# Optimization experiments

Hardware: AMD Instinct MI355X
Metric: run time of the kernel (lower is better)

## Reference

```python
import jax, jax.numpy as jnp
import numpy as np

V = 32000; D = 1024; L = 2; H = 16; KVH = 4; HD = D // H; E = 8; FF = 2048; K = 2
B = 2; S = 1024; WINDOW = 4096; THETA = 10000.0; EPS = 1e-6


def setup_inputs() -> dict:
    key = jax.random.key(0)
    ks = jax.random.split(key, 12)
    std = 0.02
    return {
        'tokens': jax.random.randint(ks[0], (B, S), 0, V),
        'tok_emb': jax.random.normal(ks[1], (V, D), jnp.float32),  # nn.Embedding default N(0,1)
        'norm1_w': jnp.ones((L, D), jnp.float32),
        'norm2_w': jnp.ones((L, D), jnp.float32),
        'wq': jax.random.normal(ks[2], (L, D, D), jnp.float32) * std,
        'wk': jax.random.normal(ks[3], (L, KVH * HD, D), jnp.float32) * std,
        'wv': jax.random.normal(ks[4], (L, KVH * HD, D), jnp.float32) * std,
        'wo': jax.random.normal(ks[5], (L, D, D), jnp.float32) * std,
        'router_w': jax.random.normal(ks[6], (L, E, D), jnp.float32) * (std / np.sqrt(D)),
        'w1': jax.random.normal(ks[7], (L, E, FF, D), jnp.float32) * std,
        'w2': jax.random.normal(ks[8], (L, E, FF, D), jnp.float32) * std,
        'w3': jax.random.normal(ks[9], (L, E, D, FF), jnp.float32) * std,
        'normf_w': jnp.ones((D,), jnp.float32),
        'head_w': jax.random.normal(ks[10], (V, D), jnp.float32) * std,
    }


def rmsnorm(x, w):
    # F.normalize(x, dim=-1, eps) * w * sqrt(d)
    n = jnp.linalg.norm(x, axis=-1, keepdims=True)
    return x / jnp.maximum(n, EPS) * w * np.float32(np.sqrt(x.shape[-1]))


def rope(x, cos, sin):
    # x: (b, s, h, hd); pairs are interleaved (even, odd) per view_as_complex
    x2 = x.reshape(x.shape[:-1] + (-1, 2))
    x0, x1 = x2[..., 0], x2[..., 1]
    o0 = x0 * cos - x1 * sin
    o1 = x0 * sin + x1 * cos
    return jnp.stack([o0, o1], axis=-1).reshape(x.shape)


def attention(x, wq, wk, wv, wo, cos, sin):
    b, s, _ = x.shape
    q = (x @ wq.T).reshape(b, s, H, HD)
    k = (x @ wk.T).reshape(b, s, KVH, HD)
    v = (x @ wv.T).reshape(b, s, KVH, HD)
    q = rope(q, cos, sin)
    k = rope(k, cos, sin)
    g = H // KVH
    k = jnp.repeat(k, g, axis=2)
    v = jnp.repeat(v, g, axis=2)
    scores = jnp.einsum('bqhd,bkhd->bhqk', q, k) / np.float32(np.sqrt(HD))
    i = jnp.arange(s)[:, None]; j = jnp.arange(s)[None, :]
    allow = (j <= i) & (i - j < WINDOW)  # causal + sliding window
    scores = jnp.where(allow, scores, -jnp.inf)
    attn = jax.nn.softmax(scores, axis=-1)
    out = jnp.einsum('bhqk,bkhd->bqhd', attn, v).reshape(b, s, D)
    return out @ wo.T


def moe(x, router_w, w1, w2, w3):
    b, s, d = x.shape
    logits = jnp.einsum('bsd,ed->bse', x, router_w)
    probs = jax.nn.softmax(logits, axis=-1)
    _, idx = jax.lax.top_k(probs, K)                      # (b, s, K)
    mask = jax.nn.one_hot(idx, E, dtype=x.dtype).sum(-2)  # (b, s, E) binary
    xt = x.reshape(-1, d)           # (T, d)
    mt = mask.reshape(-1, E)        # (T, E)
    # Dense masked dispatch: every expert computed on all tokens, combine masks to zero
    u = jnp.einsum('td,efd->etf', xt, w1)
    g = jax.nn.silu(u) * jnp.einsum('td,efd->etf', xt, w2)
    y = jnp.einsum('etf,edf->etd', g, w3)
    out = jnp.einsum('etd,te->td', y, mt).reshape(b, s, d)  # unweighted combine (per source)
    # aux losses
    z_loss = jnp.mean(jax.scipy.special.logsumexp(logits, axis=-1)) ** 2
    load = probs.sum(axis=0)  # (s, E), matching probs.sum(dim=0) in source
    load_loss = (jnp.std(load, ddof=1) / jnp.mean(load)) ** 2
    aux = 0.001 * z_loss + 0.001 * load_loss
    return out, aux


def _rope_tables(dtype):
    freqs = 1.0 / (THETA ** (np.arange(0, HD, 2, dtype=np.float32) / HD))
    ang = np.arange(S, dtype=np.float32)[:, None] * freqs[None, :]
    cos = jnp.asarray(np.cos(ang), dtype)[None, :, None, :]
    sin = jnp.asarray(np.sin(ang), dtype)[None, :, None, :]
    return cos, sin


def reference(tokens, tok_emb, norm1_w, norm2_w, wq, wk, wv, wo, router_w, w1, w2, w3, normf_w, head_w):
    x = tok_emb[tokens]  # (B, S, D)
    cos, sin = _rope_tables(x.dtype)
    attn_scale = np.float32(1.0 / np.sqrt(2.0 * L))
    aux_total = jnp.zeros((), x.dtype)
    for l in range(L):
        x = x + attn_scale * attention(rmsnorm(x, norm1_w[l]), wq[l], wk[l], wv[l], wo[l], cos, sin)
        mo, aux = moe(rmsnorm(x, norm2_w[l]), router_w[l], w1[l], w2[l], w3[l])
        x = x + mo
        aux_total = aux_total + aux
    logits = rmsnorm(x, normf_w) @ head_w.T
    return logits, aux_total
```

## Files before the change

kernel.cpp:

```cpp
#include <hip/hip_runtime.h>
#include <math.h>

#define DEV __device__ __forceinline__

using v8s = __attribute__((ext_vector_type(8))) short;
using v4f = __attribute__((ext_vector_type(4))) float;

DEV short f2bf(float f) {
    unsigned u = __float_as_uint(f);
    unsigned r = (u + 0x7fffu + ((u >> 16) & 1u)) >> 16;
    return (short)(unsigned short)r;
}
DEV float bf2f(short s) {
    return __uint_as_float(((unsigned)(unsigned short)s) << 16);
}

DEV void gload16(const short* g, short* l) {
    __builtin_amdgcn_global_load_lds((const __attribute__((address_space(1))) void*)g,
                                     (__attribute__((address_space(3))) void*)l,
                                     16, 0, 0);
}

DEV float block_sum256(float v, float* red) {
    __syncthreads();
#pragma unroll
    for (int o = 32; o >= 1; o >>= 1) v += __shfl_down(v, o, 64);
    if ((threadIdx.x & 63) == 0) red[threadIdx.x >> 6] = v;
    __syncthreads();
    return red[0] + red[1] + red[2] + red[3];
}
DEV float block_max256(float v, float* red) {
    __syncthreads();
#pragma unroll
    for (int o = 32; o >= 1; o >>= 1) v = fmaxf(v, __shfl_down(v, o, 64));
    if ((threadIdx.x & 63) == 0) red[threadIdx.x >> 6] = v;
    __syncthreads();
    return fmaxf(fmaxf(red[0], red[1]), fmaxf(red[2], red[3]));
}


__global__ __launch_bounds__(256) void conv_kernel(const float* __restrict__ src,
                                                   short* __restrict__ hi, short* __restrict__ lo,
                                                   long total4, long chunk4, long dstStride4) {
    for (long i = (long)blockIdx.x * 256 + threadIdx.x; i < total4; i += (long)gridDim.x * 256) {
        long c = i / chunk4, r = i - c * chunk4;
        long d = c * dstStride4 + r;
        float4 f = ((const float4*)src)[i];
        short h0 = f2bf(f.x), h1 = f2bf(f.y), h2 = f2bf(f.z), h3 = f2bf(f.w);
        ((ushort4*)hi)[d] = make_ushort4((unsigned short)h0, (unsigned short)h1,
                                         (unsigned short)h2, (unsigned short)h3);
        if (lo) {
            short l0 = f2bf(f.x - bf2f(h0)), l1 = f2bf(f.y - bf2f(h1));
            short l2 = f2bf(f.z - bf2f(h2)), l3 = f2bf(f.w - bf2f(h3));
            ((ushort4*)lo)[d] = make_ushort4((unsigned short)l0, (unsigned short)l1,
                                             (unsigned short)l2, (unsigned short)l3);
        }
    }
}

struct GemmP {
    const short* Ah; const short* Al;
    const short* Bh; const short* Bl;
    float* C; short* Ch; short* Cl;
    const int* cnt; const int* prefix; const int* ltok; const int* lrow;
    long strideAz, strideBz, strideCz;
    int M, N, K, lda, ldb, ldc;
    float alpha;
    int outMode;
    int gqaB;
    int attnC;
    int grouped;
    int causalSkip;
    int causalK;
    int ntiles, S, G;
};

template<bool SPLIT>
__global__ __launch_bounds__(256) void gemm_bt(GemmP p) {
    const int lid = blockIdx.x;
    const int xcd = lid & 7, sI = lid >> 3;
    const int gi = xcd + 8 * (sI / p.S);
    if (gi >= p.G) return;
    const int mt = sI % p.S;
    const int nt = gi % p.ntiles;
    const int z  = gi / p.ntiles;
    if (p.causalSkip && nt > mt) return;

    const int tid = threadIdx.x;

    int Mz = p.M;
    const int* ltokz = nullptr; const int* lrowz = nullptr; int pz = 0;
    if (p.grouped) {
        Mz = p.cnt[z]; pz = p.prefix[z];
        ltokz = p.ltok + z * 2048; lrowz = p.lrow + z * 2048;
    }
    if (mt * 128 >= Mz) return;

    long aOff = (long)z * p.strideAz;
    long bOff, cOff;
    if (p.gqaB) { int b = z >> 4, h = z & 15; bOff = (long)(b * 4 + (h >> 2)) * p.strideBz; }
    else bOff = (long)z * p.strideBz;
    if (p.attnC) { int b = z >> 4, h = z & 15; cOff = (long)b * 1048576 + h * 64; }
    else cOff = (long)z * p.strideCz;

    extern __shared__ char smem[];
    short* Ahs = (short*)smem;
    short* Bhs = Ahs + 4096;
    short* Als = Bhs + 4096;
    short* Bls = Als + 4096;

    const int lane = tid & 63, w = tid >> 6;
    const int lr = lane & 15, lg = lane >> 4;
    const int wr = w >> 1, wc = w & 1;
    const int wb = w << 9;

    v4f acc[4][4];
#pragma unroll
    for (int i = 0; i < 4; ++i)
#pragma unroll
        for (int j = 0; j < 4; ++j) { acc[i][j][0] = 0.f; acc[i][j][1] = 0.f; acc[i][j][2] = 0.f; acc[i][j][3] = 0.f; }

    const int r = tid & 127;
    const int kgA = tid >> 7;

    int am = mt * 128 + r; if (am >= Mz) am = Mz - 1;
    long arowoff;
    if (p.grouped == 1)      arowoff = (long)ltokz[am] * p.lda;
    else if (p.grouped == 2) arowoff = (long)(pz + am) * p.lda;
    else                     arowoff = aOff + (long)am * p.lda;
    int bn = nt * 128 + r; if (bn >= p.N) bn = p.N - 1;
    const long browoff = bOff + (long)bn * p.ldb;

    const short* aH = p.Ah + arowoff + kgA * 8;
    const short* bH = p.Bh + browoff + kgA * 8;
    const short* aL = SPLIT ? p.Al + arowoff + kgA * 8 : nullptr;
    const short* bL = SPLIT ? p.Bl + browoff + kgA * 8 : nullptr;

    const int kEnd = p.causalK ? min(p.K, (mt + 1) * 128) : p.K;

    for (int k0 = 0; k0 < kEnd; k0 += 32) {
        __syncthreads();
        gload16(aH + k0,      Ahs + wb);
        gload16(aH + k0 + 16, Ahs + 2048 + wb);
        gload16(bH + k0,      Bhs + wb);
        gload16(bH + k0 + 16, Bhs + 2048 + wb);
        if (SPLIT) {
            gload16(aL + k0,      Als + wb);
            gload16(aL + k0 + 16, Als + 2048 + wb);
            gload16(bL + k0,      Bls + wb);
            gload16(bL + k0 + 16, Bls + 2048 + wb);
        }
        __syncthreads();
        const int abase = lg * 1024 + (wr * 64 + lr) * 8;
        const int bbase = lg * 1024 + (wc * 64 + lr) * 8;
        v8s ah[4], bh[4];
#pragma unroll
        for (int i = 0; i < 4; ++i) {
            ah[i] = *(const v8s*)(Ahs + abase + i * 128);
            bh[i] = *(const v8s*)(Bhs + bbase + i * 128);
        }
        if constexpr (SPLIT) {
            v8s al[4], bl[4];
#pragma unroll
            for (int i = 0; i < 4; ++i) {
                al[i] = *(const v8s*)(Als + abase + i * 128);
                bl[i] = *(const v8s*)(Bls + bbase + i * 128);
            }
#pragma unroll
            for (int mi = 0; mi < 4; ++mi)
#pragma unroll
                for (int nj = 0; nj < 4; ++nj) {
                    acc[mi][nj] = __builtin_amdgcn_mfma_f32_16x16x32_bf16(ah[mi], bh[nj], acc[mi][nj], 0, 0, 0);
                    acc[mi][nj] = __builtin_amdgcn_mfma_f32_16x16x32_bf16(al[mi], bh[nj], acc[mi][nj], 0, 0, 0);
                    acc[mi][nj] = __builtin_amdgcn_mfma_f32_16x16x32_bf16(ah[mi], bl[nj], acc[mi][nj], 0, 0, 0);
                }
        } else {
#pragma unroll
            for (int mi = 0; mi < 4; ++mi)
#pragma unroll
                for (int nj = 0; nj < 4; ++nj)
                    acc[mi][nj] = __builtin_amdgcn_mfma_f32_16x16x32_bf16(ah[mi], bh[nj], acc[mi][nj], 0, 0, 0);
        }
    }

#pragma unroll
    for (int mi = 0; mi < 4; ++mi) {
        const int mrow = mt * 128 + wr * 64 + mi * 16 + lg * 4;
#pragma unroll
        for (int nj = 0; nj < 4; ++nj) {
            const int ncol = nt * 128 + wc * 64 + nj * 16 + lr;
            if (ncol < p.N) {
#pragma unroll
                for (int rr = 0; rr < 4; ++rr) {
                    const int m = mrow + rr;
                    if (m < Mz) {
                        float v = acc[mi][nj][rr] * p.alpha;
                        long crow;
                        if (p.grouped == 1) crow = pz + m;
                        else if (p.grouped == 2) crow = lrowz[m];
                        else crow = m;
                        long co = cOff + crow * (long)p.ldc + ncol;
                        if (p.outMode == 0) p.C[co] = v;
                        else if (p.outMode == 1) p.C[co] += v;
                        else {
                            short hi = f2bf(v);
                            p.Ch[co] = hi;
                            p.Cl[co] = f2bf(v - bf2f(hi));
                        }
                    }
                }
            }
        }
    }
}

__global__ __launch_bounds__(256) void embed_kernel(const int* toks, const float* emb, float* X) {
    const int t = blockIdx.x;
    const int tok = toks[t];
    const float4* s = (const float4*)(emb + (size_t)tok * 1024);
    float4* d = (float4*)(X + (size_t)t * 1024);
    d[threadIdx.x] = s[threadIdx.x];
}

__global__ __launch_bounds__(256) void rmsnorm_split(const float* X, const float* w, short* oh, short* ol) {
    __shared__ float red[4];
    const long t = blockIdx.x;
    const float* r = X + t * 1024;
    float ss = 0.f;
    for (int j = threadIdx.x; j < 1024; j += 256) { float f = r[j]; ss += f * f; }
    ss = block_sum256(ss, red);
    const float sc = 32.f / fmaxf(sqrtf(ss), 1e-6f);
    for (int j = threadIdx.x; j < 1024; j += 256) {
        float f = r[j] * sc * w[j];
        short hi = f2bf(f);
        oh[t * 1024 + j] = hi;
        ol[t * 1024 + j] = f2bf(f - bf2f(hi));
    }
}

struct RopeF { float f[32]; };

__global__ __launch_bounds__(256) void rope_q_kernel(const float* QKV, short* OH, short* OL, RopeF rf) {
    const int idx = blockIdx.x * 256 + threadIdx.x;
    const int pp = idx & 31, h = (idx >> 5) & 15, s = (idx >> 9) & 1023, b = idx >> 19;
    const float* src = QKV + ((size_t)(b * 1024 + s)) * 1536 + h * 64 + 2 * pp;
    const float x0 = src[0], x1 = src[1];
    const float ang = (float)s * rf.f[pp];
    float sn, cs; sincosf(ang, &sn, &cs);
    const float o0 = x0 * cs - x1 * sn, o1 = x0 * sn + x1 * cs;
    const size_t o = ((size_t)((b * 16 + h) * 1024 + s)) * 64 + 2 * pp;
    short h0 = f2bf(o0); OH[o] = h0; OL[o] = f2bf(o0 - bf2f(h0));
    short h1 = f2bf(o1); OH[o + 1] = h1; OL[o + 1] = f2bf(o1 - bf2f(h1));
}

__global__ __launch_bounds__(256) void rope_k_kernel(const float* QKV, short* KH, short* KL, RopeF rf) {
    const int idx = blockIdx.x * 256 + threadIdx.x;
    const int pp = idx & 31, kv = (idx >> 5) & 3, s = (idx >> 7) & 1023, b = idx >> 17;
    const float* src = QKV + ((size_t)(b * 1024 + s)) * 1536 + 1024 + kv * 64 + 2 * pp;
    const float x0 = src[0], x1 = src[1];
    const float ang = (float)s * rf.f[pp];
    float sn, cs; sincosf(ang, &sn, &cs);
    const float o0 = x0 * cs - x1 * sn, o1 = x0 * sn + x1 * cs;
    const size_t o = ((size_t)((b * 4 + kv) * 1024 + s)) * 64 + 2 * pp;
    short h0 = f2bf(o0); KH[o] = h0; KL[o] = f2bf(o0 - bf2f(h0));
    short h1 = f2bf(o1); KH[o + 1] = h1; KL[o + 1] = f2bf(o1 - bf2f(h1));
}

__global__ __launch_bounds__(256) void transpose_v_kernel(const float* QKV, short* VH, short* VL) {
    const int idx = blockIdx.x * 256 + threadIdx.x;
    const int d = idx & 63, kv = (idx >> 6) & 3, s = (idx >> 8) & 1023, b = idx >> 18;
    const float f = QKV[((size_t)(b * 1024 + s)) * 1536 + 1280 + kv * 64 + d];
    const size_t o = ((size_t)((b * 4 + kv) * 64 + d)) * 1024 + s;
    short hi = f2bf(f);
    VH[o] = hi; VL[o] = f2bf(f - bf2f(hi));
}

__global__ __launch_bounds__(256) void attn_softmax(float* SC) {
    const long row = blockIdx.x;
    const int i = (int)(row & 1023);
    float* r = SC + row * 1024;
    __shared__ float buf[1024];
    __shared__ float red[4];
    const int n = i + 1;
    for (int j = threadIdx.x; j < 1024; j += 256) buf[j] = r[j];
    __syncthreads();
    float m = -INFINITY;
    for (int j = threadIdx.x; j < n; j += 256) m = fmaxf(m, buf[j]);
    m = block_max256(m, red);
    float s = 0.f;
    for (int j = threadIdx.x; j < n; j += 256) { float e = expf(buf[j] - m); buf[j] = e; s += e; }
    s = block_sum256(s, red);
    const float inv = 1.f / s;
    short* rh = (short*)r;
    short* rl = rh + 1024;
    __syncthreads();
    for (int j = threadIdx.x; j < 1024; j += 256) {
        float pv = (j < n) ? buf[j] * inv : 0.f;
        short hi = f2bf(pv);
        rh[j] = hi;
        rl[j] = f2bf(pv - bf2f(hi));
    }
}

__global__ __launch_bounds__(256) void router_kernel(const float* X, const float* wn, const float* rw,
                                                     float* probs, float* lse, int* cnt, int* ltok, int* lrow) {
    __shared__ float xs[1024];
    __shared__ float red[4];
    __shared__ float lg[8];
    const int t = blockIdx.x;
    const float* r = X + (size_t)t * 1024;
    for (int j = threadIdx.x; j < 1024; j += 256) xs[j] = r[j];
    __syncthreads();
    float ss = 0.f;
    for (int j = threadIdx.x; j < 1024; j += 256) ss += xs[j] * xs[j];
    ss = block_sum256(ss, red);
    const float sc = 32.f / fmaxf(sqrtf(ss), 1e-6f);
    float acc[8] = {0, 0, 0, 0, 0, 0, 0, 0};
    for (int j = threadIdx.x; j < 1024; j += 256) {
        const float xv = xs[j] * wn[j];
#pragma unroll
        for (int e = 0; e < 8; ++e) acc[e] += xv * rw[e * 1024 + j];
    }
#pragma unroll
    for (int e = 0; e < 8; ++e) {
        float s = block_sum256(acc[e], red);
        if (threadIdx.x == 0) lg[e] = s * sc;
    }
    __syncthreads();
    if (threadIdx.x == 0) {
        float m = lg[0];
        for (int e = 1; e < 8; ++e) m = fmaxf(m, lg[e]);
        float ex[8], se = 0.f;
        for (int e = 0; e < 8; ++e) { ex[e] = expf(lg[e] - m); se += ex[e]; }
        const float inv = 1.f / se;
        float pr[8];
        for (int e = 0; e < 8; ++e) { pr[e] = ex[e] * inv; probs[(size_t)t * 8 + e] = pr[e]; }
        lse[t] = m + logf(se);
        int i1 = 0;
        for (int e = 1; e < 8; ++e) if (pr[e] > pr[i1]) i1 = e;
        int i2 = (i1 == 0) ? 1 : 0;
        for (int e = 0; e < 8; ++e) if (e != i1 && pr[e] > pr[i2]) i2 = e;
        int s1 = atomicAdd(&cnt[i1], 1); ltok[i1 * 2048 + s1] = t; lrow[i1 * 2048 + s1] = 2 * t;
        int s2 = atomicAdd(&cnt[i2], 1); ltok[i2 * 2048 + s2] = t; lrow[i2 * 2048 + s2] = 2 * t + 1;
    }
}

__global__ void prefix_kernel(const int* cnt, int* pref) {
    if (threadIdx.x == 0 && blockIdx.x == 0) {
        int a = 0;
        for (int e = 0; e < 8; ++e) { pref[e] = a; a += cnt[e]; }
    }
}

__global__ __launch_bounds__(256) void silu_mul(const float* U, short* HH, short* HL) {
    const long i4 = (long)blockIdx.x * 256 + threadIdx.x;
    const int f4 = (int)(i4 & 511), row = (int)(i4 >> 9);
    const float4 u = *(const float4*)(U + ((long)row << 12) + (f4 << 2));
    const float4 g = *(const float4*)(U + ((long)row << 12) + 2048 + (f4 << 2));
    float h[4];
    h[0] = (u.x / (1.f + expf(-u.x))) * g.x;
    h[1] = (u.y / (1.f + expf(-u.y))) * g.y;
    h[2] = (u.z / (1.f + expf(-u.z))) * g.z;
    h[3] = (u.w / (1.f + expf(-u.w))) * g.w;
    const long o = (long)row * 2048 + (f4 << 2);
    short h0 = f2bf(h[0]), h1 = f2bf(h[1]), h2 = f2bf(h[2]), h3 = f2bf(h[3]);
    *(ushort4*)(HH + o) = make_ushort4((unsigned short)h0, (unsigned short)h1,
                                       (unsigned short)h2, (unsigned short)h3);
    short l0 = f2bf(h[0] - bf2f(h0)), l1 = f2bf(h[1] - bf2f(h1));
    short l2 = f2bf(h[2] - bf2f(h2)), l3 = f2bf(h[3] - bf2f(h3));
    *(ushort4*)(HL + o) = make_ushort4((unsigned short)l0, (unsigned short)l1,
                                       (unsigned short)l2, (unsigned short)l3);
}

__global__ __launch_bounds__(256) void combine_kernel(float* X, const float* Y) {
    const int i4 = blockIdx.x * 256 + threadIdx.x;
    const int t = i4 >> 8, d4 = i4 & 255;
    float4 x = ((float4*)X)[i4];
    const float4 a = ((const float4*)Y)[(size_t)(2 * t) * 256 + d4];
    const float4 b = ((const float4*)Y)[(size_t)(2 * t + 1) * 256 + d4];
    x.x += a.x + b.x; x.y += a.y + b.y; x.z += a.z + b.z; x.w += a.w + b.w;
    ((float4*)X)[i4] = x;
}

__global__ __launch_bounds__(256) void aux_kernel(const float* probs, const float* lse, float* auxb, int layer) {
    __shared__ float red[4];
    float sl = 0.f;
    for (int t = threadIdx.x; t < 2048; t += 256) sl += lse[t];
    sl = block_sum256(sl, red);
    float s1 = 0.f, s2 = 0.f;
    for (int i = threadIdx.x; i < 8192; i += 256) {
        const float l = probs[i] + probs[8192 + i];
        s1 += l; s2 += l * l;
    }
    s1 = block_sum256(s1, red);
    s2 = block_sum256(s2, red);
    if (threadIdx.x == 0) {
        const float ml = sl / 2048.f;
        const float mean = s1 / 8192.f;
        const float var = fmaxf((s2 - s1 * s1 / 8192.f) / 8191.f, 0.f);
        auxb[layer] = 0.001f * (ml * ml + var / (mean * mean));
    }
}

__global__ void finalize_aux(const float* auxb, float* out) {
    if (threadIdx.x == 0 && blockIdx.x == 0)
        out[(size_t)2 * 1024 * 32000] = auxb[0] + auxb[1];
}

static void run_gemm(hipStream_t s, bool split, GemmP& p, int ntiles, int mtiles, int zdim) {
    p.ntiles = ntiles; p.S = mtiles;
    p.G = ntiles * zdim;
    int Gp = (p.G + 7) & ~7;
    long nb = (long)Gp * mtiles;
    dim3 g((unsigned)nb, 1, 1), b(256);
    if (split) gemm_bt<true><<<g, b, 32768, s>>>(p);
    else       gemm_bt<false><<<g, b, 16384, s>>>(p);
}

static void run_conv(hipStream_t s, const float* src, short* hi, short* lo,
                     long total, long chunk, long dstStride) {
    long t4 = total / 4;
    long nb = (t4 + 255) / 256; if (nb > 2048) nb = 2048;
    conv_kernel<<<(unsigned)nb, 256, 0, s>>>(src, hi, lo, t4, chunk / 4, dstStride / 4);
}

extern "C" void kernel_launch(void* const* d_in, const int* in_sizes, int n_in,
                              void* d_out, int out_size, void* d_ws, size_t ws_size,
                              hipStream_t stream) {
    (void)in_sizes; (void)n_in; (void)out_size; (void)ws_size;
    const int*   tokens = (const int*)d_in[0];
    const float* tok_emb = (const float*)d_in[1];
    const float* norm1 = (const float*)d_in[2];
    const float* norm2 = (const float*)d_in[3];
    const float* wq = (const float*)d_in[4];
    const float* wk = (const float*)d_in[5];
    const float* wv = (const float*)d_in[6];
    const float* wo = (const float*)d_in[7];
    const float* rw = (const float*)d_in[8];
    const float* w1 = (const float*)d_in[9];
    const float* w2 = (const float*)d_in[10];
    const float* w3 = (const float*)d_in[11];
    const float* normf = (const float*)d_in[12];
    const float* headw = (const float*)d_in[13];
    float* out = (float*)d_out;

    char* w = (char*)d_ws;
    const size_t MB = 1024ull * 1024ull;
    float* X    = (float*)(w + 0);
    short* XNH  = (short*)(w + 8 * MB);
    short* XNL  = (short*)(w + 12 * MB);
    short* AOH  = (short*)(w + 16 * MB);
    short* AOL  = (short*)(w + 20 * MB);
    short* QRH  = (short*)(w + 24 * MB);
    short* QRL  = (short*)(w + 28 * MB);
    short* KRH  = (short*)(w + 32 * MB);
    short* KRL  = (short*)(w + 33 * MB);
    short* VTH  = (short*)(w + 34 * MB);
    short* VTL  = (short*)(w + 35 * MB);
    float* QKV  = (float*)(w + 36 * MB);
    float* SC   = (float*)(w + 36 * MB);
    float* U    = (float*)(w + 36 * MB);
    short* HH   = (short*)(w + 100 * MB);
    short* HL   = (short*)(w + 116 * MB);
    float* Y    = (float*)(w + 132 * MB);
    float* PROBS= (float*)(w + 164 * MB);
    float* LSE  = (float*)(w + 164 * MB + 65536);
    int*   CNT  = (int*)  (w + 164 * MB + 73728);
    int*   PREF = (int*)  (w + 164 * MB + 73856);
    int*   LTOK = (int*)  (w + 164 * MB + 74240);
    int*   LROW = (int*)  (w + 164 * MB + 74240 + 65536);
    float* AUXB = (float*)(w + 164 * MB + 74240 + 131072);
    short* WQKVH = (short*)(w + 166 * MB);
    short* WQKVL = (short*)(w + 172 * MB);
    short* WOH   = (short*)(w + 178 * MB);
    short* WOL   = (short*)(w + 182 * MB);
    short* W12H  = (short*)(w + 186 * MB);
    short* W12L  = (short*)(w + 250 * MB);
    short* W3H   = (short*)(w + 314 * MB);
    short* W3L   = (short*)(w + 346 * MB);
    short* HDH   = (short*)(w + 378 * MB);

    RopeF rf;
    for (int i = 0; i < 32; ++i) {
        float t = (float)pow(10000.0, (double)(2 * i) / 64.0);
        rf.f[i] = 1.0f / t;
    }

    for (int l = 0; l < 2; ++l) {
        long qo = (long)l * 1572864;
        run_conv(stream, wq + (long)l * 1048576, WQKVH + qo,           WQKVL + qo,           1048576, 1048576, 1048576);
        run_conv(stream, wk + (long)l * 262144,  WQKVH + qo + 1048576, WQKVL + qo + 1048576, 262144,  262144,  262144);
        run_conv(stream, wv + (long)l * 262144,  WQKVH + qo + 1310720, WQKVL + qo + 1310720, 262144,  262144,  262144);
    }
    run_conv(stream, wo, WOH, WOL, 2097152, 2097152, 2097152);
    run_conv(stream, headw, HDH, nullptr, 32768000, 32768000, 32768000);

    embed_kernel<<<2048, 256, 0, stream>>>(tokens, tok_emb, X);

    for (int l = 0; l < 2; ++l) {
        const bool msp = (l == 0);
        run_conv(stream, w1 + (long)l * 16777216, W12H,           msp ? W12L : nullptr,           16777216, 2097152, 4194304);
        run_conv(stream, w2 + (long)l * 16777216, W12H + 2097152, msp ? W12L + 2097152 : nullptr, 16777216, 2097152, 4194304);
        run_conv(stream, w3 + (long)l * 16777216, W3H,            msp ? W3L : nullptr,            16777216, 16777216, 16777216);

        rmsnorm_split<<<2048, 256, 0, stream>>>(X, norm1 + l * 1024, XNH, XNL);

        { GemmP p = {}; p.Ah = XNH; p.Al = XNL; p.Bh = WQKVH + (long)l * 1572864; p.Bl = WQKVL + (long)l * 1572864;
          p.C = QKV; p.M = 2048; p.N = 1536; p.K = 1024; p.lda = 1024; p.ldb = 1024; p.ldc = 1536; p.alpha = 1.f;
          run_gemm(stream, true, p, 12, 16, 1); }

        rope_q_kernel<<<4096, 256, 0, stream>>>(QKV, QRH, QRL, rf);
        rope_k_kernel<<<1024, 256, 0, stream>>>(QKV, KRH, KRL, rf);
        transpose_v_kernel<<<2048, 256, 0, stream>>>(QKV, VTH, VTL);

        { GemmP p = {}; p.Ah = QRH; p.Al = QRL; p.Bh = KRH; p.Bl = KRL; p.C = SC;
          p.M = 1024; p.N = 1024; p.K = 64; p.lda = 64; p.ldb = 64; p.ldc = 1024;
          p.strideAz = 65536; p.strideBz = 65536; p.strideCz = 1048576;
          p.alpha = 0.125f; p.gqaB = 1; p.causalSkip = 1;
          run_gemm(stream, true, p, 8, 8, 32); }

        attn_softmax<<<32768, 256, 0, stream>>>(SC);

        { GemmP p = {}; p.Ah = (short*)SC; p.Al = (short*)SC + 1024; p.Bh = VTH; p.Bl = VTL; p.Ch = AOH; p.Cl = AOL;
          p.M = 1024; p.N = 64; p.K = 1024; p.lda = 2048; p.ldb = 1024; p.ldc = 1024;
          p.strideAz = 2097152; p.strideBz = 65536;
          p.alpha = 1.f; p.gqaB = 1; p.attnC = 1; p.causalK = 1; p.outMode = 2;
          run_gemm(stream, true, p, 1, 8, 32); }

        { GemmP p = {}; p.Ah = AOH; p.Al = AOL; p.Bh = WOH + (long)l * 1048576; p.Bl = WOL + (long)l * 1048576; p.C = X;
          p.M = 2048; p.N = 1024; p.K = 1024; p.lda = 1024; p.ldb = 1024; p.ldc = 1024;
          p.alpha = 0.5f; p.outMode = 1;
          run_gemm(stream, true, p, 8, 16, 1); }

        rmsnorm_split<<<2048, 256, 0, stream>>>(X, norm2 + l * 1024, XNH, XNL);
        hipMemsetAsync(CNT, 0, 8 * sizeof(int), stream);
        router_kernel<<<2048, 256, 0, stream>>>(X, norm2 + l * 1024, rw + (size_t)l * 8 * 1024,
                                                PROBS, LSE, CNT, LTOK, LROW);
        prefix_kernel<<<1, 64, 0, stream>>>(CNT, PREF);

        { GemmP p = {}; p.Ah = XNH; p.Al = XNL; p.Bh = W12H; p.Bl = W12L; p.C = U;
          p.M = 2048; p.N = 4096; p.K = 1024; p.lda = 1024; p.ldb = 1024; p.ldc = 4096;
          p.strideBz = 4194304; p.alpha = 1.f; p.grouped = 1;
          p.cnt = CNT; p.prefix = PREF; p.ltok = LTOK; p.lrow = LROW;
          run_gemm(stream, msp, p, 32, 16, 8); }
        silu_mul<<<8192, 256, 0, stream>>>(U, HH, HL);
        { GemmP p = {}; p.Ah = HH; p.Al = HL; p.Bh = W3H; p.Bl = W3L; p.C = Y;
          p.M = 2048; p.N = 1024; p.K = 2048; p.lda = 2048; p.ldb = 2048; p.ldc = 1024;
          p.strideBz = 2097152; p.alpha = 1.f; p.grouped = 2;
          p.cnt = CNT; p.prefix = PREF; p.ltok = LTOK; p.lrow = LROW;
          run_gemm(stream, msp, p, 8, 16, 8); }
        combine_kernel<<<2048, 256, 0, stream>>>(X, Y);
        aux_kernel<<<1, 256, 0, stream>>>(PROBS, LSE, AUXB, l);
    }

    rmsnorm_split<<<2048, 256, 0, stream>>>(X, normf, XNH, XNL);
    { GemmP p = {}; p.Ah = XNH; p.Bh = HDH; p.C = out;
      p.M = 2048; p.N = 32000; p.K = 1024; p.lda = 1024; p.ldb = 1024; p.ldc = 32000; p.alpha = 1.f;
      run_gemm(stream, false, p, 250, 16, 1); }
    finalize_aux<<<1, 1, 0, stream>>>(AUXB, out);
}
```

Before: 2.319 ms.

## Pre-tile B operands into LDS-ready panels and stage A through registers

The weight conversion kernels, K-rope and V-transpose now write their bf16 hi/lo outputs in a 128-row panel layout that matches the GEMM's shared-memory tile. Each block can then fetch its B tile with fully contiguous global_load_lds transfers instead of strided row gathers. The A tile is now loaded into registers before the barrier and stored to LDS afterwards, so the global latency overlaps the previous iteration. This reshapes several producer kernels and buffer offsets together. It risks layout mismatches, for example the V padding zero-writes and the changed strides.

```diff
diff --git a/kernel.cpp b/kernel.cpp
--- a/kernel.cpp
+++ b/kernel.cpp
@@ -39,21 +39,34 @@
 }
 
 
-__global__ __launch_bounds__(256) void conv_kernel(const float* __restrict__ src,
-                                                   short* __restrict__ hi, short* __restrict__ lo,
-                                                   long total4, long chunk4, long dstStride4) {
-    for (long i = (long)blockIdx.x * 256 + threadIdx.x; i < total4; i += (long)gridDim.x * 256) {
-        long c = i / chunk4, r = i - c * chunk4;
-        long d = c * dstStride4 + r;
-        float4 f = ((const float4*)src)[i];
-        short h0 = f2bf(f.x), h1 = f2bf(f.y), h2 = f2bf(f.z), h3 = f2bf(f.w);
-        ((ushort4*)hi)[d] = make_ushort4((unsigned short)h0, (unsigned short)h1,
-                                         (unsigned short)h2, (unsigned short)h3);
+__global__ __launch_bounds__(256) void conv_tile(const float* __restrict__ src,
+                                                 short* __restrict__ hi, short* __restrict__ lo,
+                                                 long nGroups, int Kg, long chunkRows, long chunkPanelStride) {
+    const long panelElems = 128L * Kg * 8;
+    for (long idx = (long)blockIdx.x * 256 + threadIdx.x; idx < nGroups; idx += (long)gridDim.x * 256) {
+        long rrow = idx / Kg; int g = (int)(idx - rrow * Kg);
+        int kblk = g >> 2, kg = g & 3;
+        long c = rrow / chunkRows; int ri = (int)(rrow - c * chunkRows);
+        long panel = c * chunkPanelStride + (ri >> 7);
+        int row = ri & 127;
+        long dst = panel * panelElems + (long)kblk * 4096 + kg * 1024 + row * 8;
+        const float4 f0 = ((const float4*)src)[idx * 2];
+        const float4 f1 = ((const float4*)src)[idx * 2 + 1];
+        short h0 = f2bf(f0.x), h1 = f2bf(f0.y), h2 = f2bf(f0.z), h3 = f2bf(f0.w);
+        short h4 = f2bf(f1.x), h5 = f2bf(f1.y), h6 = f2bf(f1.z), h7 = f2bf(f1.w);
+        *(ushort4*)(hi + dst)     = make_ushort4((unsigned short)h0, (unsigned short)h1,
+                                                 (unsigned short)h2, (unsigned short)h3);
+        *(ushort4*)(hi + dst + 4) = make_ushort4((unsigned short)h4, (unsigned short)h5,
+                                                 (unsigned short)h6, (unsigned short)h7);
         if (lo) {
-            short l0 = f2bf(f.x - bf2f(h0)), l1 = f2bf(f.y - bf2f(h1));
-            short l2 = f2bf(f.z - bf2f(h2)), l3 = f2bf(f.w - bf2f(h3));
-            ((ushort4*)lo)[d] = make_ushort4((unsigned short)l0, (unsigned short)l1,
-                                             (unsigned short)l2, (unsigned short)l3);
+            short l0 = f2bf(f0.x - bf2f(h0)), l1 = f2bf(f0.y - bf2f(h1));
+            short l2 = f2bf(f0.z - bf2f(h2)), l3 = f2bf(f0.w - bf2f(h3));
+            short l4 = f2bf(f1.x - bf2f(h4)), l5 = f2bf(f1.y - bf2f(h5));
+            short l6 = f2bf(f1.z - bf2f(h6)), l7 = f2bf(f1.w - bf2f(h7));
+            *(ushort4*)(lo + dst)     = make_ushort4((unsigned short)l0, (unsigned short)l1,
+                                                     (unsigned short)l2, (unsigned short)l3);
+            *(ushort4*)(lo + dst + 4) = make_ushort4((unsigned short)l4, (unsigned short)l5,
+                                                     (unsigned short)l6, (unsigned short)l7);
         }
     }
 }
@@ -64,7 +77,7 @@
     float* C; short* Ch; short* Cl;
     const int* cnt; const int* prefix; const int* ltok; const int* lrow;
     long strideAz, strideBz, strideCz;
-    int M, N, K, lda, ldb, ldc;
+    int M, N, K, lda, ldc;
     float alpha;
     int outMode;
     int gqaB;
@@ -112,7 +125,6 @@
     const int lane = tid & 63, w = tid >> 6;
     const int lr = lane & 15, lg = lane >> 4;
     const int wr = w >> 1, wc = w & 1;
-    const int wb = w << 9;
 
     v4f acc[4][4];
 #pragma unroll
@@ -122,34 +134,40 @@
 
     const int r = tid & 127;
     const int kgA = tid >> 7;
-
     int am = mt * 128 + r; if (am >= Mz) am = Mz - 1;
     long arowoff;
     if (p.grouped == 1)      arowoff = (long)ltokz[am] * p.lda;
     else if (p.grouped == 2) arowoff = (long)(pz + am) * p.lda;
     else                     arowoff = aOff + (long)am * p.lda;
-    int bn = nt * 128 + r; if (bn >= p.N) bn = p.N - 1;
-    const long browoff = bOff + (long)bn * p.ldb;
-
-    const short* aH = p.Ah + arowoff + kgA * 8;
-    const short* bH = p.Bh + browoff + kgA * 8;
-    const short* aL = SPLIT ? p.Al + arowoff + kgA * 8 : nullptr;
-    const short* bL = SPLIT ? p.Bl + browoff + kgA * 8 : nullptr;
+    const short* aH = p.Ah + arowoff + kgA * 16;
+    const short* aL = SPLIT ? p.Al + arowoff + kgA * 16 : nullptr;
+    short* sA0 = Ahs + (kgA * 256 + r) * 8;
+    short* sA1 = sA0 + 1024;
+    short* sA0l = Als + (kgA * 256 + r) * 8;
+    short* sA1l = sA0l + 1024;
+
+    const short* bks  = p.Bh + bOff + (long)nt * 128 * p.K + (long)w * 1024 + lane * 8;
+    const short* bksL = SPLIT ? p.Bl + bOff + (long)nt * 128 * p.K + (long)w * 1024 + lane * 8 : nullptr;
+    short* dB  = Bhs + w * 1024;
+    short* dBl = Bls + w * 1024;
 
     const int kEnd = p.causalK ? min(p.K, (mt + 1) * 128) : p.K;
 
     for (int k0 = 0; k0 < kEnd; k0 += 32) {
+        const long kb = (long)k0 * 128;
+        uint4 a0 = *(const uint4*)(aH + k0);
+        uint4 a1 = *(const uint4*)(aH + k0 + 8);
+        uint4 a0l, a1l;
+        if (SPLIT) { a0l = *(const uint4*)(aL + k0); a1l = *(const uint4*)(aL + k0 + 8); }
         __syncthreads();
-        gload16(aH + k0,      Ahs + wb);
-        gload16(aH + k0 + 16, Ahs + 2048 + wb);
-        gload16(bH + k0,      Bhs + wb);
-        gload16(bH + k0 + 16, Bhs + 2048 + wb);
+        gload16(bks + kb,       dB);
+        gload16(bks + kb + 512, dB + 512);
         if (SPLIT) {
-            gload16(aL + k0,      Als + wb);
-            gload16(aL + k0 + 16, Als + 2048 + wb);
-            gload16(bL + k0,      Bls + wb);
-            gload16(bL + k0 + 16, Bls + 2048 + wb);
+            gload16(bksL + kb,       dBl);
+            gload16(bksL + kb + 512, dBl + 512);
         }
+        *(uint4*)sA0 = a0; *(uint4*)sA1 = a1;
+        if (SPLIT) { *(uint4*)sA0l = a0l; *(uint4*)sA1l = a1l; }
         __syncthreads();
         const int abase = lg * 1024 + (wr * 64 + lr) * 8;
         const int bbase = lg * 1024 + (wc * 64 + lr) * 8;
@@ -261,18 +279,24 @@
     const float ang = (float)s * rf.f[pp];
     float sn, cs; sincosf(ang, &sn, &cs);
     const float o0 = x0 * cs - x1 * sn, o1 = x0 * sn + x1 * cs;
-    const size_t o = ((size_t)((b * 4 + kv) * 1024 + s)) * 64 + 2 * pp;
-    short h0 = f2bf(o0); KH[o] = h0; KL[o] = f2bf(o0 - bf2f(h0));
-    short h1 = f2bf(o1); KH[o + 1] = h1; KL[o + 1] = f2bf(o1 - bf2f(h1));
+    const int z = b * 4 + kv, d = 2 * pp;
+    const long off = (long)z * 65536 + (long)(s >> 7) * 8192
+                   + ((long)(d >> 5) << 12) + ((long)((d >> 3) & 3) << 10)
+                   + ((long)(s & 127) << 3) + (d & 7);
+    short h0 = f2bf(o0); KH[off] = h0; KL[off] = f2bf(o0 - bf2f(h0));
+    short h1 = f2bf(o1); KH[off + 1] = h1; KL[off + 1] = f2bf(o1 - bf2f(h1));
 }
 
 __global__ __launch_bounds__(256) void transpose_v_kernel(const float* QKV, short* VH, short* VL) {
     const int idx = blockIdx.x * 256 + threadIdx.x;
     const int d = idx & 63, kv = (idx >> 6) & 3, s = (idx >> 8) & 1023, b = idx >> 18;
     const float f = QKV[((size_t)(b * 1024 + s)) * 1536 + 1280 + kv * 64 + d];
-    const size_t o = ((size_t)((b * 4 + kv) * 64 + d)) * 1024 + s;
+    const int z = b * 4 + kv;
+    const long off = (long)z * 131072 + ((long)(s >> 5) << 12) + ((long)((s >> 3) & 3) << 10)
+                   + ((long)d << 3) + (s & 7);
     short hi = f2bf(f);
-    VH[o] = hi; VL[o] = f2bf(f - bf2f(hi));
+    VH[off] = hi; VL[off] = f2bf(f - bf2f(hi));
+    VH[off + 512] = 0; VL[off + 512] = 0;
 }
 
 __global__ __launch_bounds__(256) void attn_softmax(float* SC) {
@@ -417,11 +441,11 @@
     else       gemm_bt<false><<<g, b, 16384, s>>>(p);
 }
 
-static void run_conv(hipStream_t s, const float* src, short* hi, short* lo,
-                     long total, long chunk, long dstStride) {
-    long t4 = total / 4;
-    long nb = (t4 + 255) / 256; if (nb > 2048) nb = 2048;
-    conv_kernel<<<(unsigned)nb, 256, 0, s>>>(src, hi, lo, t4, chunk / 4, dstStride / 4);
+static void run_tile(hipStream_t s, const float* src, short* hi, short* lo,
+                     long rows, int K, long chunkRows, long chunkPanelStride) {
+    long groups = rows * (K / 8);
+    long nb = (groups + 255) / 256; if (nb > 2048) nb = 2048;
+    conv_tile<<<(unsigned)nb, 256, 0, s>>>(src, hi, lo, groups, K / 8, chunkRows, chunkPanelStride);
 }
 
 extern "C" void kernel_launch(void* const* d_in, const int* in_sizes, int n_in,
@@ -449,36 +473,36 @@
     float* X    = (float*)(w + 0);
     short* XNH  = (short*)(w + 8 * MB);
     short* XNL  = (short*)(w + 12 * MB);
-    short* AOH  = (short*)(w + 16 * MB);
-    short* AOL  = (short*)(w + 20 * MB);
-    short* QRH  = (short*)(w + 24 * MB);
-    short* QRL  = (short*)(w + 28 * MB);
-    short* KRH  = (short*)(w + 32 * MB);
-    short* KRL  = (short*)(w + 33 * MB);
-    short* VTH  = (short*)(w + 34 * MB);
-    short* VTL  = (short*)(w + 35 * MB);
-    float* QKV  = (float*)(w + 36 * MB);
-    float* SC   = (float*)(w + 36 * MB);
-    float* U    = (float*)(w + 36 * MB);
-    short* HH   = (short*)(w + 100 * MB);
-    short* HL   = (short*)(w + 116 * MB);
-    float* Y    = (float*)(w + 132 * MB);
-    float* PROBS= (float*)(w + 164 * MB);
-    float* LSE  = (float*)(w + 164 * MB + 65536);
-    int*   CNT  = (int*)  (w + 164 * MB + 73728);
-    int*   PREF = (int*)  (w + 164 * MB + 73856);
-    int*   LTOK = (int*)  (w + 164 * MB + 74240);
-    int*   LROW = (int*)  (w + 164 * MB + 74240 + 65536);
-    float* AUXB = (float*)(w + 164 * MB + 74240 + 131072);
-    short* WQKVH = (short*)(w + 166 * MB);
-    short* WQKVL = (short*)(w + 172 * MB);
-    short* WOH   = (short*)(w + 178 * MB);
-    short* WOL   = (short*)(w + 182 * MB);
-    short* W12H  = (short*)(w + 186 * MB);
-    short* W12L  = (short*)(w + 250 * MB);
-    short* W3H   = (short*)(w + 314 * MB);
-    short* W3L   = (short*)(w + 346 * MB);
-    short* HDH   = (short*)(w + 378 * MB);
+    short* QRH  = (short*)(w + 16 * MB);
+    short* QRL  = (short*)(w + 20 * MB);
+    short* AOH  = QRH;
+    short* AOL  = QRL;
+    short* KRH  = (short*)(w + 24 * MB);
+    short* KRL  = (short*)(w + 25 * MB);
+    short* VTH  = (short*)(w + 26 * MB);
+    short* VTL  = (short*)(w + 28 * MB);
+    float* QKV  = (float*)(w + 32 * MB);
+    float* SC   = (float*)(w + 32 * MB);
+    float* U    = (float*)(w + 32 * MB);
+    short* HH   = (short*)(w + 96 * MB);
+    short* HL   = (short*)(w + 112 * MB);
+    float* Y    = (float*)(w + 128 * MB);
+    float* PROBS= (float*)(w + 160 * MB);
+    float* LSE  = (float*)(w + 160 * MB + 65536);
+    int*   CNT  = (int*)  (w + 160 * MB + 73728);
+    int*   PREF = (int*)  (w + 160 * MB + 73856);
+    int*   LTOK = (int*)  (w + 160 * MB + 74240);
+    int*   LROW = (int*)  (w + 160 * MB + 74240 + 65536);
+    float* AUXB = (float*)(w + 160 * MB + 74240 + 131072);
+    short* WQKVH = (short*)(w + 162 * MB);
+    short* WQKVL = (short*)(w + 168 * MB);
+    short* WOH   = (short*)(w + 174 * MB);
+    short* WOL   = (short*)(w + 178 * MB);
+    short* W12H  = (short*)(w + 182 * MB);
+    short* W12L  = (short*)(w + 246 * MB);
+    short* W3H   = (short*)(w + 310 * MB);
+    short* W3L   = (short*)(w + 342 * MB);
+    short* HDH   = (short*)(w + 374 * MB);
 
     RopeF rf;
     for (int i = 0; i < 32; ++i) {
@@ -488,25 +512,25 @@
 
     for (int l = 0; l < 2; ++l) {
         long qo = (long)l * 1572864;
-        run_conv(stream, wq + (long)l * 1048576, WQKVH + qo,           WQKVL + qo,           1048576, 1048576, 1048576);
-        run_conv(stream, wk + (long)l * 262144,  WQKVH + qo + 1048576, WQKVL + qo + 1048576, 262144,  262144,  262144);
-        run_conv(stream, wv + (long)l * 262144,  WQKVH + qo + 1310720, WQKVL + qo + 1310720, 262144,  262144,  262144);
-    }
-    run_conv(stream, wo, WOH, WOL, 2097152, 2097152, 2097152);
-    run_conv(stream, headw, HDH, nullptr, 32768000, 32768000, 32768000);
+        run_tile(stream, wq + (long)l * 1048576, WQKVH + qo,           WQKVL + qo,           1024, 1024, 1024, 8);
+        run_tile(stream, wk + (long)l * 262144,  WQKVH + qo + 1048576, WQKVL + qo + 1048576, 256, 1024, 256, 2);
+        run_tile(stream, wv + (long)l * 262144,  WQKVH + qo + 1310720, WQKVL + qo + 1310720, 256, 1024, 256, 2);
+    }
+    run_tile(stream, wo, WOH, WOL, 2048, 1024, 2048, 16);
+    run_tile(stream, headw, HDH, nullptr, 32000, 1024, 32000, 250);
 
     embed_kernel<<<2048, 256, 0, stream>>>(tokens, tok_emb, X);
 
     for (int l = 0; l < 2; ++l) {
         const bool msp = (l == 0);
-        run_conv(stream, w1 + (long)l * 16777216, W12H,           msp ? W12L : nullptr,           16777216, 2097152, 4194304);
-        run_conv(stream, w2 + (long)l * 16777216, W12H + 2097152, msp ? W12L + 2097152 : nullptr, 16777216, 2097152, 4194304);
-        run_conv(stream, w3 + (long)l * 16777216, W3H,            msp ? W3L : nullptr,            16777216, 16777216, 16777216);
+        run_tile(stream, w1 + (long)l * 16777216, W12H,           msp ? W12L : nullptr,           16384, 1024, 2048, 32);
+        run_tile(stream, w2 + (long)l * 16777216, W12H + 2097152, msp ? W12L + 2097152 : nullptr, 16384, 1024, 2048, 32);
+        run_tile(stream, w3 + (long)l * 16777216, W3H,            msp ? W3L : nullptr,            8192, 2048, 8192, 64);
 
         rmsnorm_split<<<2048, 256, 0, stream>>>(X, norm1 + l * 1024, XNH, XNL);
 
         { GemmP p = {}; p.Ah = XNH; p.Al = XNL; p.Bh = WQKVH + (long)l * 1572864; p.Bl = WQKVL + (long)l * 1572864;
-          p.C = QKV; p.M = 2048; p.N = 1536; p.K = 1024; p.lda = 1024; p.ldb = 1024; p.ldc = 1536; p.alpha = 1.f;
+          p.C = QKV; p.M = 2048; p.N = 1536; p.K = 1024; p.lda = 1024; p.ldc = 1536; p.alpha = 1.f;
           run_gemm(stream, true, p, 12, 16, 1); }
 
         rope_q_kernel<<<4096, 256, 0, stream>>>(QKV, QRH, QRL, rf);
@@ -514,7 +538,7 @@
         transpose_v_kernel<<<2048, 256, 0, stream>>>(QKV, VTH, VTL);
 
         { GemmP p = {}; p.Ah = QRH; p.Al = QRL; p.Bh = KRH; p.Bl = KRL; p.C = SC;
-          p.M = 1024; p.N = 1024; p.K = 64; p.lda = 64; p.ldb = 64; p.ldc = 1024;
+          p.M = 1024; p.N = 1024; p.K = 64; p.lda = 64; p.ldc = 1024;
           p.strideAz = 65536; p.strideBz = 65536; p.strideCz = 1048576;
           p.alpha = 0.125f; p.gqaB = 1; p.causalSkip = 1;
           run_gemm(stream, true, p, 8, 8, 32); }
@@ -522,13 +546,13 @@
         attn_softmax<<<32768, 256, 0, stream>>>(SC);
 
         { GemmP p = {}; p.Ah = (short*)SC; p.Al = (short*)SC + 1024; p.Bh = VTH; p.Bl = VTL; p.Ch = AOH; p.Cl = AOL;
-          p.M = 1024; p.N = 64; p.K = 1024; p.lda = 2048; p.ldb = 1024; p.ldc = 1024;
-          p.strideAz = 2097152; p.strideBz = 65536;
+          p.M = 1024; p.N = 64; p.K = 1024; p.lda = 2048; p.ldc = 1024;
+          p.strideAz = 2097152; p.strideBz = 131072;
           p.alpha = 1.f; p.gqaB = 1; p.attnC = 1; p.causalK = 1; p.outMode = 2;
           run_gemm(stream, true, p, 1, 8, 32); }
 
         { GemmP p = {}; p.Ah = AOH; p.Al = AOL; p.Bh = WOH + (long)l * 1048576; p.Bl = WOL + (long)l * 1048576; p.C = X;
-          p.M = 2048; p.N = 1024; p.K = 1024; p.lda = 1024; p.ldb = 1024; p.ldc = 1024;
+          p.M = 2048; p.N = 1024; p.K = 1024; p.lda = 1024; p.ldc = 1024;
           p.alpha = 0.5f; p.outMode = 1;
           run_gemm(stream, true, p, 8, 16, 1); }
 
@@ -539,13 +563,13 @@
         prefix_kernel<<<1, 64, 0, stream>>>(CNT, PREF);
 
         { GemmP p = {}; p.Ah = XNH; p.Al = XNL; p.Bh = W12H; p.Bl = W12L; p.C = U;
-          p.M = 2048; p.N = 4096; p.K = 1024; p.lda = 1024; p.ldb = 1024; p.ldc = 4096;
+          p.M = 2048; p.N = 4096; p.K = 1024; p.lda = 1024; p.ldc = 4096;
           p.strideBz = 4194304; p.alpha = 1.f; p.grouped = 1;
           p.cnt = CNT; p.prefix = PREF; p.ltok = LTOK; p.lrow = LROW;
           run_gemm(stream, msp, p, 32, 16, 8); }
         silu_mul<<<8192, 256, 0, stream>>>(U, HH, HL);
         { GemmP p = {}; p.Ah = HH; p.Al = HL; p.Bh = W3H; p.Bl = W3L; p.C = Y;
-          p.M = 2048; p.N = 1024; p.K = 2048; p.lda = 2048; p.ldb = 2048; p.ldc = 1024;
+          p.M = 2048; p.N = 1024; p.K = 2048; p.lda = 2048; p.ldc = 1024;
           p.strideBz = 2097152; p.alpha = 1.f; p.grouped = 2;
           p.cnt = CNT; p.prefix = PREF; p.ltok = LTOK; p.lrow = LROW;
           run_gemm(stream, msp, p, 8, 16, 8); }
@@ -555,7 +579,7 @@
 
     rmsnorm_split<<<2048, 256, 0, stream>>>(X, normf, XNH, XNL);
     { GemmP p = {}; p.Ah = XNH; p.Bh = HDH; p.C = out;
-      p.M = 2048; p.N = 32000; p.K = 1024; p.lda = 1024; p.ldb = 1024; p.ldc = 32000; p.alpha = 1.f;
+      p.M = 2048; p.N = 32000; p.K = 1024; p.lda = 1024; p.ldc = 32000; p.alpha = 1.f;
       run_gemm(stream, false, p, 250, 16, 1); }
     finalize_aux<<<1, 1, 0, stream>>>(AUXB, out);
 }
```

After: 2.310 ms. About the same (-0.4%).
